# Kernel tuning notes

Measured on AMD Instinct MI355X. Metric: run time of the kernel, lower is better.

The kernel has to match this reference:

```python
import jax, jax.numpy as jnp
import numpy as np

B, N, C = 4, 2048, 1024
H = 16
HD = C // H
SCALE = HD ** -0.5


def setup_inputs() -> dict:
    key = jax.random.key(0)
    k1, k2, k3 = jax.random.split(key, 3)
    x = jax.random.normal(k1, (B, N, C), dtype=jnp.float32)
    qkv_w = jax.random.normal(k2, (3 * C, C), dtype=jnp.float32) * (C ** -0.5)
    proj_w = jax.random.normal(k3, (C, C), dtype=jnp.float32) * (C ** -0.5)
    proj_b = jnp.zeros((C,), dtype=jnp.float32)
    return {"x": x, "qkv_w": qkv_w, "proj_w": proj_w, "proj_b": proj_b}


def reference(x, qkv_w, proj_w, proj_b):
    b, n, c = x.shape
    # qkv: [B, N, 3C] -> [3, B, H, N, HD]
    qkv = jnp.einsum('bnc,dc->bnd', x, qkv_w)
    qkv = qkv.reshape(b, n, 3, H, c // H).transpose(2, 0, 3, 1, 4)
    q, k, v = qkv[0] * SCALE, qkv[1], qkv[2]
    # attention scores [B, H, N, N]
    attn = jnp.einsum('bhqd,bhkd->bhqk', q, k)
    attn = jax.nn.softmax(attn, axis=-1)
    out = jnp.einsum('bhqk,bhkd->bhqd', attn, v)  # [B, H, N, HD]
    out = out.transpose(0, 2, 1, 3).reshape(b, n, c)
    out = jnp.einsum('bnc,dc->bnd', out, proj_w) + proj_b
    return out
```

## Files before the change

kernel.cpp:

```cpp
#include <hip/hip_runtime.h>
#include <math.h>

#define B_  4
#define N_  2048
#define C_  1024
#define H_  16
#define HD_ 64
#define QSCALE_ 0.18033688011112042f
#define THR_ 8.0f

typedef float f32x4 __attribute__((ext_vector_type(4)));
typedef short short8 __attribute__((ext_vector_type(8)));
typedef unsigned short ushort8 __attribute__((ext_vector_type(8)));

__device__ inline unsigned short f2bf(float f) {
    union { float f; unsigned u; } v; v.f = f;
    unsigned r = v.u + 0x7fffu + ((v.u >> 16) & 1u);
    return (unsigned short)(r >> 16);
}

#define GLD16(gptr, lptr) \
    __builtin_amdgcn_global_load_lds((const __attribute__((address_space(1))) unsigned int*)(gptr), \
                                     (__attribute__((address_space(3))) unsigned int*)(lptr), 16, 0, 0)

__global__ __launch_bounds__(256) void cast_bf16_k(const float* __restrict__ in,
                                                   unsigned short* __restrict__ out, int n8) {
    int i = blockIdx.x * 256 + threadIdx.x;
    if (i >= n8) return;
    const float4* p = (const float4*)in + (size_t)i * 2;
    float4 a = p[0], b = p[1];
    ushort8 o;
    o[0]=f2bf(a.x); o[1]=f2bf(a.y); o[2]=f2bf(a.z); o[3]=f2bf(a.w);
    o[4]=f2bf(b.x); o[5]=f2bf(b.y); o[6]=f2bf(b.z); o[7]=f2bf(b.w);
    *((ushort8*)out + i) = o;
}

__device__ inline void gemm128_core(const unsigned short* __restrict__ A,
                                    const unsigned short* __restrict__ Bm,
                                    int m0, int n0, int K,
                                    unsigned short* sA, unsigned short* sB,
                                    f32x4 acc[4][4])
{
    const int tid = threadIdx.x;
    const int lane = tid & 63, w = tid >> 6;
    const int lg = lane >> 4, lr = lane & 15;
    const int wr = (w >> 1) * 64, wc = (w & 1) * 64;
    const int srow = tid >> 2, schunk = tid & 3;
    const unsigned wbase = (unsigned)(tid & 192) * 16;

    for (int k0 = 0; k0 < K; k0 += 32) {
        __syncthreads();
        GLD16(&A[(size_t)(m0 + srow) * K + k0 + schunk * 8],      (char*)sA + wbase);
        GLD16(&A[(size_t)(m0 + srow + 64) * K + k0 + schunk * 8], (char*)sA + 4096 + wbase);
        GLD16(&Bm[(size_t)(n0 + srow) * K + k0 + schunk * 8],      (char*)sB + wbase);
        GLD16(&Bm[(size_t)(n0 + srow + 64) * K + k0 + schunk * 8], (char*)sB + 4096 + wbase);
        __syncthreads();
        short8 af[4], bf[4];
#pragma unroll
        for (int i = 0; i < 4; ++i) {
            af[i] = *(const short8*)&sA[(wr + i*16 + lr) * 32 + lg * 8];
            bf[i] = *(const short8*)&sB[(wc + i*16 + lr) * 32 + lg * 8];
        }
#pragma unroll
        for (int i = 0; i < 4; ++i)
#pragma unroll
            for (int j = 0; j < 4; ++j)
                acc[i][j] = __builtin_amdgcn_mfma_f32_16x16x32_bf16(af[i], bf[j], acc[i][j], 0, 0, 0);
    }
}

__global__ __launch_bounds__(256) void qkv_gemm_k(const unsigned short* __restrict__ x,
                                                  const unsigned short* __restrict__ w,
                                                  unsigned short* __restrict__ qkv) {
    __shared__ unsigned short sA[128 * 32];
    __shared__ unsigned short sB[128 * 32];
    f32x4 acc[4][4];
    f32x4 z = {0.f, 0.f, 0.f, 0.f};
#pragma unroll
    for (int i = 0; i < 4; ++i)
#pragma unroll
        for (int j = 0; j < 4; ++j) acc[i][j] = z;

    const int m0 = blockIdx.x * 128, n0 = blockIdx.y * 128;
    gemm128_core(x, w, m0, n0, C_, sA, sB, acc);

    const int lane = threadIdx.x & 63, w4 = threadIdx.x >> 6;
    const int lg = lane >> 4, lr = lane & 15;
    const int wr = (w4 >> 1) * 64, wc = (w4 & 1) * 64;
#pragma unroll
    for (int mi = 0; mi < 4; ++mi)
#pragma unroll
        for (int ni = 0; ni < 4; ++ni) {
            int nc = n0 + wc + ni * 16 + lr;
            int type = nc >> 10, c = nc & 1023;
            int hh = c >> 6, hd = c & 63;
            float sc = (type == 0) ? QSCALE_ : 1.0f;
#pragma unroll
            for (int r = 0; r < 4; ++r) {
                int tok = m0 + wr + mi * 16 + lg * 4 + r;
                int bb = tok >> 11, n = tok & (N_ - 1);
                qkv[(((size_t)type * B_ + bb) * H_ + hh) * ((size_t)N_ * HD_) + (size_t)n * HD_ + hd]
                    = f2bf(acc[mi][ni][r] * sc);
            }
        }
}

__global__ __launch_bounds__(256) void vtrans_k(const unsigned short* __restrict__ qkv,
                                                unsigned short* __restrict__ vt) {
    __shared__ unsigned short st[64 * 72];
    const int tid = threadIdx.x;
    const int n0 = blockIdx.x * 64;
    const int bh = blockIdx.y;
    const unsigned short* V = qkv + (size_t)2 * B_ * H_ * N_ * HD_ + (size_t)bh * N_ * HD_;
    unsigned short* VT = vt + (size_t)bh * HD_ * N_;
    const int r = tid >> 2, c = tid & 3;
    ushort8 v0 = *(const ushort8*)&V[(size_t)(n0 + r) * HD_ + c * 8];
    ushort8 v1 = *(const ushort8*)&V[(size_t)(n0 + r) * HD_ + (c + 4) * 8];
    *(ushort8*)&st[r * 72 + c * 8] = v0;
    *(ushort8*)&st[r * 72 + (c + 4) * 8] = v1;
    __syncthreads();
#pragma unroll
    for (int cc = 0; cc < 2; ++cc) {
        int ch = c + cc * 4;
        ushort8 o;
#pragma unroll
        for (int j = 0; j < 8; ++j) o[j] = st[(ch * 8 + j) * 72 + r];
        *(ushort8*)&VT[(size_t)r * N_ + n0 + ch * 8] = o;
    }
}

__global__ __launch_bounds__(256) void attn_k(const unsigned short* __restrict__ qkv,
                                              const unsigned short* __restrict__ vt,
                                              unsigned short* __restrict__ aout) {
    __shared__ __align__(16) char smem[34816];
    unsigned short* sK = (unsigned short*)smem;
    unsigned short* sV = (unsigned short*)(smem + 8192);
    unsigned short* sP = (unsigned short*)(smem + 16384);

    const int tid = threadIdx.x, lane = tid & 63, w = tid >> 6;
    const int lg = lane >> 4, lr = lane & 15;
    const int qt = blockIdx.x, h = blockIdx.y, b = blockIdx.z;
    const size_t plane = (size_t)B_ * H_ * N_ * HD_;
    const size_t bhoff = ((size_t)b * H_ + h) * ((size_t)N_ * HD_);
    const unsigned short* Q = qkv + bhoff;
    const unsigned short* K = qkv + plane + bhoff;
    const unsigned short* VT = vt + ((size_t)b * H_ + h) * ((size_t)HD_ * N_);

    const int qbase = qt * 128 + w * 32;
    short8 qf[2][2];
#pragma unroll
    for (int rb = 0; rb < 2; ++rb)
#pragma unroll
        for (int ks = 0; ks < 2; ++ks)
            qf[rb][ks] = *(const short8*)&Q[(size_t)(qbase + rb * 16 + lr) * HD_ + ks * 32 + lg * 8];

    f32x4 acc[2][4];
    float m_run[2], l_run[2];
    f32x4 z = {0.f, 0.f, 0.f, 0.f};
#pragma unroll
    for (int rb = 0; rb < 2; ++rb) {
#pragma unroll
        for (int df = 0; df < 4; ++df) acc[rb][df] = z;
        m_run[rb] = -1e30f; l_run[rb] = 0.f;
    }

    const int srow = tid >> 3, schunk = tid & 7;
    const int scs = schunk ^ (srow & 7);
    const unsigned wbase = (unsigned)(tid & 192) * 16;

    const int pswz = (lr & 8) << 1;
    const int prow = (w * 32 + lr) * 72;

    for (int kt = 0; kt < N_ / 64; ++kt) {
        const int k0 = kt * 64;
        __syncthreads();
        GLD16(&K[(size_t)(k0 + srow) * HD_ + scs * 8],       smem + wbase);
        GLD16(&K[(size_t)(k0 + srow + 32) * HD_ + scs * 8],  smem + 4096 + wbase);
        GLD16(&VT[(size_t)srow * N_ + k0 + scs * 8],         smem + 8192 + wbase);
        GLD16(&VT[(size_t)(srow + 32) * N_ + k0 + scs * 8],  smem + 12288 + wbase);
        __syncthreads();

        f32x4 S[2][4];
        {
            short8 kf[4][2];
#pragma unroll
            for (int kb = 0; kb < 4; ++kb)
#pragma unroll
                for (int ks = 0; ks < 2; ++ks)
                    kf[kb][ks] = *(const short8*)&sK[(kb * 16 + lr) * 64 + (((ks * 4 + lg) ^ (lr & 7)) * 8)];
#pragma unroll
            for (int rb = 0; rb < 2; ++rb)
#pragma unroll
                for (int kb = 0; kb < 4; ++kb) {
                    f32x4 t = __builtin_amdgcn_mfma_f32_16x16x32_bf16(kf[kb][0], qf[rb][0], z, 0, 0, 0);
                    S[rb][kb] = __builtin_amdgcn_mfma_f32_16x16x32_bf16(kf[kb][1], qf[rb][1], t, 0, 0, 0);
                }
        }

        float mx[2];
#pragma unroll
        for (int rb = 0; rb < 2; ++rb) {
            float m0 = fmaxf(fmaxf(S[rb][0][0], S[rb][0][1]), fmaxf(S[rb][0][2], S[rb][0][3]));
#pragma unroll
            for (int kb = 1; kb < 4; ++kb) {
                float m1 = fmaxf(fmaxf(S[rb][kb][0], S[rb][kb][1]), fmaxf(S[rb][kb][2], S[rb][kb][3]));
                m0 = fmaxf(m0, m1);
            }
            m0 = fmaxf(m0, __shfl_xor(m0, 16));
            m0 = fmaxf(m0, __shfl_xor(m0, 32));
            mx[rb] = m0;
        }
        bool need = (mx[0] > m_run[0] + THR_) || (mx[1] > m_run[1] + THR_);
        if (__any(need)) {
#pragma unroll
            for (int rb = 0; rb < 2; ++rb) {
                float mnew = fmaxf(m_run[rb], mx[rb]);
                float al = __builtin_amdgcn_exp2f(m_run[rb] - mnew);
                m_run[rb] = mnew;
                l_run[rb] *= al;
#pragma unroll
                for (int df = 0; df < 4; ++df)
#pragma unroll
                    for (int r = 0; r < 4; ++r) acc[rb][df][r] *= al;
            }
        }
#pragma unroll
        for (int rb = 0; rb < 2; ++rb) {
            float rs = 0.f;
#pragma unroll
            for (int kb = 0; kb < 4; ++kb) {
#pragma unroll
                for (int r = 0; r < 4; ++r) {
                    float p = __builtin_amdgcn_exp2f(S[rb][kb][r] - m_run[rb]);
                    S[rb][kb][r] = p;
                    rs += p;
                }
                unsigned u0 = (unsigned)f2bf(S[rb][kb][0]) | ((unsigned)f2bf(S[rb][kb][1]) << 16);
                unsigned u1 = (unsigned)f2bf(S[rb][kb][2]) | ((unsigned)f2bf(S[rb][kb][3]) << 16);
                int base = prow + rb * 16 * 72;
                *(unsigned*)&sP[base + ((kb * 16 + lg * 4 + 0) ^ pswz)] = u0;
                *(unsigned*)&sP[base + ((kb * 16 + lg * 4 + 2) ^ pswz)] = u1;
            }
            rs += __shfl_xor(rs, 16);
            rs += __shfl_xor(rs, 32);
            l_run[rb] += rs;
        }

        {
            short8 pa[2][2], va[4][2];
#pragma unroll
            for (int rb = 0; rb < 2; ++rb)
#pragma unroll
                for (int ks = 0; ks < 2; ++ks)
                    pa[rb][ks] = *(const short8*)&sP[prow + rb * 16 * 72 + ((ks * 32 + lg * 8) ^ pswz)];
#pragma unroll
            for (int df = 0; df < 4; ++df)
#pragma unroll
                for (int ks = 0; ks < 2; ++ks)
                    va[df][ks] = *(const short8*)&sV[(df * 16 + lr) * 64 + (((ks * 4 + lg) ^ (lr & 7)) * 8)];
#pragma unroll
            for (int rb = 0; rb < 2; ++rb)
#pragma unroll
                for (int df = 0; df < 4; ++df) {
                    acc[rb][df] = __builtin_amdgcn_mfma_f32_16x16x32_bf16(va[df][0], pa[rb][0], acc[rb][df], 0, 0, 0);
                    acc[rb][df] = __builtin_amdgcn_mfma_f32_16x16x32_bf16(va[df][1], pa[rb][1], acc[rb][df], 0, 0, 0);
                }
        }
    }

    __syncthreads();
    unsigned short* epi = (unsigned short*)smem;
#pragma unroll
    for (int rb = 0; rb < 2; ++rb) {
        float inv = 1.0f / l_run[rb];
#pragma unroll
        for (int df = 0; df < 4; ++df)
#pragma unroll
            for (int r = 0; r < 4; ++r)
                epi[(w * 32 + rb * 16 + lr) * 72 + df * 16 + lg * 4 + r] = f2bf(acc[rb][df][r] * inv);
    }
    __syncthreads();
#pragma unroll
    for (int it = 0; it < 4; ++it) {
        int id = it * 256 + tid;
        int t = id >> 3, dc = id & 7;
        ushort8 o = *(const ushort8*)&epi[t * 72 + dc * 8];
        *(ushort8*)&aout[((size_t)b * N_ + qt * 128 + t) * C_ + h * HD_ + dc * 8] = o;
    }
}

__global__ __launch_bounds__(256) void proj_gemm_k(const unsigned short* __restrict__ a,
                                                   const unsigned short* __restrict__ w,
                                                   const float* __restrict__ bias,
                                                   float* __restrict__ out) {
    __shared__ unsigned short sA[128 * 32];
    __shared__ unsigned short sB[128 * 32];
    f32x4 acc[4][4];
    f32x4 z = {0.f, 0.f, 0.f, 0.f};
#pragma unroll
    for (int i = 0; i < 4; ++i)
#pragma unroll
        for (int j = 0; j < 4; ++j) acc[i][j] = z;

    const int m0 = blockIdx.x * 128, n0 = blockIdx.y * 128;
    gemm128_core(a, w, m0, n0, C_, sA, sB, acc);

    const int lane = threadIdx.x & 63, w4 = threadIdx.x >> 6;
    const int lg = lane >> 4, lr = lane & 15;
    const int wr = (w4 >> 1) * 64, wc = (w4 & 1) * 64;
#pragma unroll
    for (int mi = 0; mi < 4; ++mi)
#pragma unroll
        for (int ni = 0; ni < 4; ++ni) {
            int ch = n0 + wc + ni * 16 + lr;
            float bv = bias[ch];
#pragma unroll
            for (int r = 0; r < 4; ++r) {
                int tok = m0 + wr + mi * 16 + lg * 4 + r;
                out[(size_t)tok * C_ + ch] = acc[mi][ni][r] + bv;
            }
        }
}

extern "C" void kernel_launch(void* const* d_in, const int* in_sizes, int n_in,
                              void* d_out, int out_size, void* d_ws, size_t ws_size,
                              hipStream_t stream) {
    const float* x      = (const float*)d_in[0];
    const float* qkv_w  = (const float*)d_in[1];
    const float* proj_w = (const float*)d_in[2];
    const float* proj_b = (const float*)d_in[3];
    float* out = (float*)d_out;

    unsigned short* x_bf    = (unsigned short*)d_ws;
    unsigned short* wqkv_bf = x_bf + (size_t)B_ * N_ * C_;
    unsigned short* wproj_bf= wqkv_bf + (size_t)3 * C_ * C_;
    unsigned short* qkv     = wproj_bf + (size_t)C_ * C_;
    unsigned short* vt      = qkv + (size_t)3 * B_ * H_ * N_ * HD_;
    unsigned short* attn    = vt + (size_t)B_ * H_ * HD_ * N_;

    const int nx = B_ * N_ * C_;
    const int nwq = 3 * C_ * C_;
    const int nwp = C_ * C_;

    cast_bf16_k<<<nx / 8 / 256, 256, 0, stream>>>(x, x_bf, nx / 8);
    cast_bf16_k<<<nwq / 8 / 256, 256, 0, stream>>>(qkv_w, wqkv_bf, nwq / 8);
    cast_bf16_k<<<nwp / 8 / 256, 256, 0, stream>>>(proj_w, wproj_bf, nwp / 8);

    qkv_gemm_k<<<dim3((B_ * N_) / 128, (3 * C_) / 128), 256, 0, stream>>>(x_bf, wqkv_bf, qkv);
    vtrans_k<<<dim3(N_ / 64, B_ * H_), 256, 0, stream>>>(qkv, vt);
    attn_k<<<dim3(N_ / 128, H_, B_), 256, 0, stream>>>(qkv, vt, attn);
    proj_gemm_k<<<dim3((B_ * N_) / 128, C_ / 128), 256, 0, stream>>>(attn, wproj_bf, proj_b, out);
}
```

Measured before the change: 321.0 us.

## Rework attention to 32x32 MFMA and keep P in registers via permlane swap

Result: faster. 297.5 us (-7.3%).

```diff
diff --git a/kernel.cpp b/kernel.cpp
--- a/kernel.cpp
+++ b/kernel.cpp
@@ -9,14 +9,22 @@
 #define QSCALE_ 0.18033688011112042f
 #define THR_ 8.0f
 
-typedef float f32x4 __attribute__((ext_vector_type(4)));
+typedef float f32x4  __attribute__((ext_vector_type(4)));
+typedef float f32x16 __attribute__((ext_vector_type(16)));
 typedef short short8 __attribute__((ext_vector_type(8)));
 typedef unsigned short ushort8 __attribute__((ext_vector_type(8)));
+typedef unsigned int uint2v __attribute__((ext_vector_type(2)));
 
 __device__ inline unsigned short f2bf(float f) {
     union { float f; unsigned u; } v; v.f = f;
     unsigned r = v.u + 0x7fffu + ((v.u >> 16) & 1u);
     return (unsigned short)(r >> 16);
+}
+
+__device__ inline unsigned cvtpk_bf16(float lo, float hi) {
+    unsigned r;
+    asm("v_cvt_pk_bf16_f32 %0, %1, %2" : "=v"(r) : "v"(lo), "v"(hi));
+    return r;
 }
 
 #define GLD16(gptr, lptr) \
@@ -132,13 +140,12 @@
 __global__ __launch_bounds__(256) void attn_k(const unsigned short* __restrict__ qkv,
                                               const unsigned short* __restrict__ vt,
                                               unsigned short* __restrict__ aout) {
-    __shared__ __align__(16) char smem[34816];
+    __shared__ __align__(16) char smem[18432];
     unsigned short* sK = (unsigned short*)smem;
     unsigned short* sV = (unsigned short*)(smem + 8192);
-    unsigned short* sP = (unsigned short*)(smem + 16384);
 
     const int tid = threadIdx.x, lane = tid & 63, w = tid >> 6;
-    const int lg = lane >> 4, lr = lane & 15;
+    const int q31 = lane & 31, hi = lane >> 5, l7 = lane & 7;
     const int qt = blockIdx.x, h = blockIdx.y, b = blockIdx.z;
     const size_t plane = (size_t)B_ * H_ * N_ * HD_;
     const size_t bhoff = ((size_t)b * H_ + h) * ((size_t)N_ * HD_);
@@ -147,29 +154,20 @@
     const unsigned short* VT = vt + ((size_t)b * H_ + h) * ((size_t)HD_ * N_);
 
     const int qbase = qt * 128 + w * 32;
-    short8 qf[2][2];
-#pragma unroll
-    for (int rb = 0; rb < 2; ++rb)
-#pragma unroll
-        for (int ks = 0; ks < 2; ++ks)
-            qf[rb][ks] = *(const short8*)&Q[(size_t)(qbase + rb * 16 + lr) * HD_ + ks * 32 + lg * 8];
-
-    f32x4 acc[2][4];
-    float m_run[2], l_run[2];
-    f32x4 z = {0.f, 0.f, 0.f, 0.f};
-#pragma unroll
-    for (int rb = 0; rb < 2; ++rb) {
-#pragma unroll
-        for (int df = 0; df < 4; ++df) acc[rb][df] = z;
-        m_run[rb] = -1e30f; l_run[rb] = 0.f;
-    }
+
+    short8 qf[4];
+#pragma unroll
+    for (int ks = 0; ks < 4; ++ks)
+        qf[ks] = *(const short8*)&Q[(size_t)(qbase + q31) * HD_ + ks * 16 + hi * 8];
+
+    f32x16 O0, O1;
+#pragma unroll
+    for (int r = 0; r < 16; ++r) { O0[r] = 0.f; O1[r] = 0.f; }
+    float m_run = -1e30f, l_run = 0.f;
 
     const int srow = tid >> 3, schunk = tid & 7;
     const int scs = schunk ^ (srow & 7);
     const unsigned wbase = (unsigned)(tid & 192) * 16;
-
-    const int pswz = (lr & 8) << 1;
-    const int prow = (w * 32 + lr) * 72;
 
     for (int kt = 0; kt < N_ / 64; ++kt) {
         const int k0 = kt * 64;
@@ -180,112 +178,97 @@
         GLD16(&VT[(size_t)(srow + 32) * N_ + k0 + scs * 8],  smem + 12288 + wbase);
         __syncthreads();
 
-        f32x4 S[2][4];
-        {
-            short8 kf[4][2];
-#pragma unroll
-            for (int kb = 0; kb < 4; ++kb)
-#pragma unroll
-                for (int ks = 0; ks < 2; ++ks)
-                    kf[kb][ks] = *(const short8*)&sK[(kb * 16 + lr) * 64 + (((ks * 4 + lg) ^ (lr & 7)) * 8)];
-#pragma unroll
-            for (int rb = 0; rb < 2; ++rb)
-#pragma unroll
-                for (int kb = 0; kb < 4; ++kb) {
-                    f32x4 t = __builtin_amdgcn_mfma_f32_16x16x32_bf16(kf[kb][0], qf[rb][0], z, 0, 0, 0);
-                    S[rb][kb] = __builtin_amdgcn_mfma_f32_16x16x32_bf16(kf[kb][1], qf[rb][1], t, 0, 0, 0);
-                }
-        }
-
-        float mx[2];
-#pragma unroll
-        for (int rb = 0; rb < 2; ++rb) {
-            float m0 = fmaxf(fmaxf(S[rb][0][0], S[rb][0][1]), fmaxf(S[rb][0][2], S[rb][0][3]));
-#pragma unroll
-            for (int kb = 1; kb < 4; ++kb) {
-                float m1 = fmaxf(fmaxf(S[rb][kb][0], S[rb][kb][1]), fmaxf(S[rb][kb][2], S[rb][kb][3]));
-                m0 = fmaxf(m0, m1);
-            }
-            m0 = fmaxf(m0, __shfl_xor(m0, 16));
-            m0 = fmaxf(m0, __shfl_xor(m0, 32));
-            mx[rb] = m0;
-        }
-        bool need = (mx[0] > m_run[0] + THR_) || (mx[1] > m_run[1] + THR_);
+        f32x16 S0, S1;
+#pragma unroll
+        for (int r = 0; r < 16; ++r) { S0[r] = 0.f; S1[r] = 0.f; }
+#pragma unroll
+        for (int ks = 0; ks < 4; ++ks) {
+            short8 kfa = *(const short8*)&sK[(size_t)q31 * 64 + (((2*ks + hi) ^ l7) * 8)];
+            short8 kfb = *(const short8*)&sK[(size_t)(32 + q31) * 64 + (((2*ks + hi) ^ l7) * 8)];
+            S0 = __builtin_amdgcn_mfma_f32_32x32x16_bf16(kfa, qf[ks], S0, 0, 0, 0);
+            S1 = __builtin_amdgcn_mfma_f32_32x32x16_bf16(kfb, qf[ks], S1, 0, 0, 0);
+        }
+
+        float t[16];
+#pragma unroll
+        for (int r = 0; r < 16; ++r) t[r] = fmaxf(S0[r], S1[r]);
+#pragma unroll
+        for (int s = 8; s > 0; s >>= 1)
+#pragma unroll
+            for (int r = 0; r < s; ++r) t[r] = fmaxf(t[r], t[r + s]);
+        float mx = fmaxf(t[0], __shfl_xor(t[0], 32));
+
+        bool need = mx > m_run + THR_;
         if (__any(need)) {
-#pragma unroll
-            for (int rb = 0; rb < 2; ++rb) {
-                float mnew = fmaxf(m_run[rb], mx[rb]);
-                float al = __builtin_amdgcn_exp2f(m_run[rb] - mnew);
-                m_run[rb] = mnew;
-                l_run[rb] *= al;
-#pragma unroll
-                for (int df = 0; df < 4; ++df)
-#pragma unroll
-                    for (int r = 0; r < 4; ++r) acc[rb][df][r] *= al;
-            }
-        }
-#pragma unroll
-        for (int rb = 0; rb < 2; ++rb) {
-            float rs = 0.f;
-#pragma unroll
-            for (int kb = 0; kb < 4; ++kb) {
-#pragma unroll
-                for (int r = 0; r < 4; ++r) {
-                    float p = __builtin_amdgcn_exp2f(S[rb][kb][r] - m_run[rb]);
-                    S[rb][kb][r] = p;
-                    rs += p;
-                }
-                unsigned u0 = (unsigned)f2bf(S[rb][kb][0]) | ((unsigned)f2bf(S[rb][kb][1]) << 16);
-                unsigned u1 = (unsigned)f2bf(S[rb][kb][2]) | ((unsigned)f2bf(S[rb][kb][3]) << 16);
-                int base = prow + rb * 16 * 72;
-                *(unsigned*)&sP[base + ((kb * 16 + lg * 4 + 0) ^ pswz)] = u0;
-                *(unsigned*)&sP[base + ((kb * 16 + lg * 4 + 2) ^ pswz)] = u1;
-            }
-            rs += __shfl_xor(rs, 16);
-            rs += __shfl_xor(rs, 32);
-            l_run[rb] += rs;
-        }
-
-        {
-            short8 pa[2][2], va[4][2];
-#pragma unroll
-            for (int rb = 0; rb < 2; ++rb)
-#pragma unroll
-                for (int ks = 0; ks < 2; ++ks)
-                    pa[rb][ks] = *(const short8*)&sP[prow + rb * 16 * 72 + ((ks * 32 + lg * 8) ^ pswz)];
-#pragma unroll
-            for (int df = 0; df < 4; ++df)
-#pragma unroll
-                for (int ks = 0; ks < 2; ++ks)
-                    va[df][ks] = *(const short8*)&sV[(df * 16 + lr) * 64 + (((ks * 4 + lg) ^ (lr & 7)) * 8)];
-#pragma unroll
-            for (int rb = 0; rb < 2; ++rb)
-#pragma unroll
-                for (int df = 0; df < 4; ++df) {
-                    acc[rb][df] = __builtin_amdgcn_mfma_f32_16x16x32_bf16(va[df][0], pa[rb][0], acc[rb][df], 0, 0, 0);
-                    acc[rb][df] = __builtin_amdgcn_mfma_f32_16x16x32_bf16(va[df][1], pa[rb][1], acc[rb][df], 0, 0, 0);
-                }
+            float mnew = fmaxf(m_run, mx);
+            float al = __builtin_amdgcn_exp2f(m_run - mnew);
+            m_run = mnew;
+            l_run *= al;
+            O0 *= al;
+            O1 *= al;
+        }
+        float rs0 = 0.f, rs1 = 0.f;
+#pragma unroll
+        for (int r = 0; r < 16; ++r) {
+            float p0 = __builtin_amdgcn_exp2f(S0[r] - m_run);
+            float p1 = __builtin_amdgcn_exp2f(S1[r] - m_run);
+            S0[r] = p0; S1[r] = p1;
+            rs0 += p0; rs1 += p1;
+        }
+        float rs = rs0 + rs1;
+        rs += __shfl_xor(rs, 32);
+        l_run += rs;
+
+        short8 pB[4];
+#pragma unroll
+        for (int ksk = 0; ksk < 4; ++ksk) {
+            const int off = (ksk & 1) * 8;
+            float e0, e1, e2, e3, e4, e5, e6, e7;
+            if (ksk < 2) { e0=S0[off+0]; e1=S0[off+1]; e2=S0[off+2]; e3=S0[off+3];
+                           e4=S0[off+4]; e5=S0[off+5]; e6=S0[off+6]; e7=S0[off+7]; }
+            else         { e0=S1[off+0]; e1=S1[off+1]; e2=S1[off+2]; e3=S1[off+3];
+                           e4=S1[off+4]; e5=S1[off+5]; e6=S1[off+6]; e7=S1[off+7]; }
+            unsigned a_ = cvtpk_bf16(e0, e1);
+            unsigned b_ = cvtpk_bf16(e4, e5);
+            unsigned c_ = cvtpk_bf16(e2, e3);
+            unsigned d_ = cvtpk_bf16(e6, e7);
+            uint2v r1 = __builtin_amdgcn_permlane32_swap(a_, b_, false, false);
+            uint2v r2 = __builtin_amdgcn_permlane32_swap(c_, d_, false, false);
+            union { unsigned u[4]; short8 s; } uu;
+            uu.u[0] = r1[0]; uu.u[1] = r2[0]; uu.u[2] = r1[1]; uu.u[3] = r2[1];
+            pB[ksk] = uu.s;
+        }
+
+#pragma unroll
+        for (int ksk = 0; ksk < 4; ++ksk) {
+            short8 va0 = *(const short8*)&sV[(size_t)q31 * 64 + (((2*ksk + hi) ^ l7) * 8)];
+            short8 va1 = *(const short8*)&sV[(size_t)(32 + q31) * 64 + (((2*ksk + hi) ^ l7) * 8)];
+            O0 = __builtin_amdgcn_mfma_f32_32x32x16_bf16(va0, pB[ksk], O0, 0, 0, 0);
+            O1 = __builtin_amdgcn_mfma_f32_32x32x16_bf16(va1, pB[ksk], O1, 0, 0, 0);
         }
     }
 
     __syncthreads();
     unsigned short* epi = (unsigned short*)smem;
-#pragma unroll
-    for (int rb = 0; rb < 2; ++rb) {
-        float inv = 1.0f / l_run[rb];
-#pragma unroll
-        for (int df = 0; df < 4; ++df)
-#pragma unroll
-            for (int r = 0; r < 4; ++r)
-                epi[(w * 32 + rb * 16 + lr) * 72 + df * 16 + lg * 4 + r] = f2bf(acc[rb][df][r] * inv);
+    {
+        float inv = 1.0f / l_run;
+        const int row = w * 32 + q31;
+#pragma unroll
+        for (int g = 0; g < 4; ++g) {
+            int col0 = 8 * g + 4 * hi;
+            *(unsigned*)&epi[row * 72 + col0]      = cvtpk_bf16(O0[4*g+0]*inv, O0[4*g+1]*inv);
+            *(unsigned*)&epi[row * 72 + col0 + 2]  = cvtpk_bf16(O0[4*g+2]*inv, O0[4*g+3]*inv);
+            *(unsigned*)&epi[row * 72 + 32 + col0]     = cvtpk_bf16(O1[4*g+0]*inv, O1[4*g+1]*inv);
+            *(unsigned*)&epi[row * 72 + 32 + col0 + 2] = cvtpk_bf16(O1[4*g+2]*inv, O1[4*g+3]*inv);
+        }
     }
     __syncthreads();
 #pragma unroll
     for (int it = 0; it < 4; ++it) {
         int id = it * 256 + tid;
-        int t = id >> 3, dc = id & 7;
-        ushort8 o = *(const ushort8*)&epi[t * 72 + dc * 8];
-        *(ushort8*)&aout[((size_t)b * N_ + qt * 128 + t) * C_ + h * HD_ + dc * 8] = o;
+        int tk = id >> 3, dc = id & 7;
+        ushort8 o = *(const ushort8*)&epi[tk * 72 + dc * 8];
+        *(ushort8*)&aout[((size_t)b * N_ + qt * 128 + tk) * C_ + h * HD_ + dc * 8] = o;
     }
 }
 
```
